# Performance work log

Measured on AMD Instinct MI355X. Metric: run time of the kernel, lower is better.

## Reference

```python
import jax, jax.numpy as jnp
import numpy as np

TEMPERATURE = 2.0
RAD2DEG = 180.0 / np.pi


def _safe_norm(diff, axis=-1):
    # L2 norm with zero (sub)gradient at 0, matching torch's convention and
    # avoiding NaNs on the (later-discarded) diagonal of pairwise distances.
    d2 = jnp.sum(diff * diff, axis=axis)
    pos = d2 > 0
    return jnp.where(pos, jnp.sqrt(jnp.where(pos, d2, 1.0)), 0.0)


def _rot6d_to_matrix(d6):
    # pytorch3d.transforms.rotation_6d_to_matrix: Gram-Schmidt on two 3-vectors.
    a1, a2 = d6[..., :3], d6[..., 3:6]
    b1 = a1 / jnp.linalg.norm(a1, axis=-1, keepdims=True)
    a2p = a2 - jnp.sum(b1 * a2, axis=-1, keepdims=True) * b1
    b2 = a2p / jnp.linalg.norm(a2p, axis=-1, keepdims=True)
    b3 = jnp.cross(b1, b2)
    return jnp.stack([b1, b2, b3], axis=-2)  # [n, 3, 3], rows b1,b2,b3


def _pose_error(pose):
    rot = _rot6d_to_matrix(pose[:, :6])                    # [n,3,3]
    div = jnp.power(jnp.linalg.det(rot), 1.0 / 3.0)[:, None, None]
    rot = rot / div
    t = pose[:, 6:]                                        # [n,3]
    # trace(rot_i @ rot_j^T) = sum_ab rot_i[a,b]*rot_j[a,b]
    r_trace = jnp.einsum('iab,jab->ij', rot, rot)          # [n,n]
    cos_theta = (r_trace - 1.0) / 2.0
    theta = jnp.arccos(jnp.clip(cos_theta, -1.0, 1.0)) * RAD2DEG
    shift = _safe_norm(t[:, None, :] - t[None, :, :]) * 100.0
    return theta, shift


def reference(features, labels):
    n = features.shape[0]
    theta_diffs, shift_diffs = _pose_error(labels)

    # FeatureSimilarity('l2'): -||f_i - f_j|| / t
    logits = -_safe_norm(features[:, None, :] - features[None, :, :]) / TEMPERATURE
    logits = logits - jax.lax.stop_gradient(jnp.max(logits, axis=1, keepdims=True))
    exp_logits = jnp.exp(logits)

    # Drop diagonal -> [n, n-1], preserving ascending column order (masked_select).
    cols = jnp.arange(n - 1)
    jidx = cols[None, :] + (cols[None, :] >= jnp.arange(n)[:, None]).astype(cols.dtype)
    take = lambda x: jnp.take_along_axis(x, jidx, axis=1)
    L = take(logits)          # [n, n-1]
    E = take(exp_logits)      # [n, n-1]
    TD = take(theta_diffs)    # [n, n-1]
    SD = take(shift_diffs)    # [n, n-1]

    # Vectorize the k-loop: M[i,k,j] = diffs[i,j] >= diffs[i,k]
    mt = TD[:, None, :] >= TD[:, :, None]                 # [n, n-1, n-1]
    ms = SD[:, None, :] >= SD[:, :, None]
    denom_t = jnp.sum(jnp.where(mt, E[:, None, :], 0.0), axis=-1)  # [n, n-1]
    denom_s = jnp.sum(jnp.where(ms, E[:, None, :], 0.0), axis=-1)

    pos_log_probs = (2.0 * L - jnp.log(denom_t) - jnp.log(denom_s)) / 2.0
    return -jnp.sum(pos_log_probs) / (n * (n - 1))


def setup_inputs() -> dict:
    key = jax.random.key(0)
    k1, k2 = jax.random.split(key)
    features = jax.random.normal(k1, (512, 256), dtype=jnp.float32)
    labels = jax.random.normal(k2, (512, 9), dtype=jnp.float32)
    return {"features": features, "labels": labels}
```

## Files before the change

### kernel.cpp

```cpp
#include <hip/hip_runtime.h>
#include <math.h>

#define N 512
#define D 256
#define ITILE 2
#define TPB 512

__constant__ float kRad2Deg = 57.29577951308232f;

__global__ void prep_kernel(const float* __restrict__ labels,
                            float* __restrict__ rot,
                            float* __restrict__ tvec) {
    int i = blockIdx.x * blockDim.x + threadIdx.x;
    if (i >= N) return;
    const float* p = labels + i * 9;
    float a1x = p[0], a1y = p[1], a1z = p[2];
    float a2x = p[3], a2y = p[4], a2z = p[5];
    float n1 = sqrtf(a1x * a1x + a1y * a1y + a1z * a1z);
    float b1x = a1x / n1, b1y = a1y / n1, b1z = a1z / n1;
    float dp = b1x * a2x + b1y * a2y + b1z * a2z;
    float cx = a2x - dp * b1x, cy = a2y - dp * b1y, cz = a2z - dp * b1z;
    float n2 = sqrtf(cx * cx + cy * cy + cz * cz);
    float b2x = cx / n2, b2y = cy / n2, b2z = cz / n2;
    float b3x = b1y * b2z - b1z * b2y;
    float b3y = b1z * b2x - b1x * b2z;
    float b3z = b1x * b2y - b1y * b2x;
    float det = b1x * (b2y * b3z - b2z * b3y)
              - b1y * (b2x * b3z - b2z * b3x)
              + b1z * (b2x * b3y - b2y * b3x);
    float inv = 1.0f / cbrtf(det);
    float* r = rot + i * 9;
    r[0] = b1x * inv; r[1] = b1y * inv; r[2] = b1z * inv;
    r[3] = b2x * inv; r[4] = b2y * inv; r[5] = b2z * inv;
    r[6] = b3x * inv; r[7] = b3y * inv; r[8] = b3z * inv;
    tvec[i * 3 + 0] = p[6];
    tvec[i * 3 + 1] = p[7];
    tvec[i * 3 + 2] = p[8];
}

__global__ __launch_bounds__(TPB) void fused_kernel(
        const float* __restrict__ f,
        const float* __restrict__ rot,
        const float* __restrict__ tvec,
        float* __restrict__ acc) {
    __shared__ __attribute__((aligned(16))) float lds_fi[ITILE * D];
    __shared__ __attribute__((aligned(16))) float E2[ITILE][N];
    __shared__ __attribute__((aligned(16))) float TD2[ITILE][N];
    __shared__ __attribute__((aligned(16))) float SD2[ITILE][N];
    __shared__ float red[TPB / 64];

    const int j  = threadIdx.x;
    const int i0 = blockIdx.x * ITILE;

    lds_fi[j] = f[i0 * D + j];
    __syncthreads();

    float d2[ITILE];
#pragma unroll
    for (int r = 0; r < ITILE; ++r) d2[r] = 0.0f;

    const float4* __restrict__ fj4 = (const float4*)(f + j * D);
#pragma unroll 8
    for (int kk = 0; kk < D / 4; ++kk) {
        float4 v = fj4[kk];
#pragma unroll
        for (int r = 0; r < ITILE; ++r) {
            const float4 fi = *(const float4*)&lds_fi[r * D + kk * 4];
            float dx = fi.x - v.x, dy = fi.y - v.y;
            float dz = fi.z - v.z, dw = fi.w - v.w;
            d2[r] += dx * dx + dy * dy + dz * dz + dw * dw;
        }
    }

    float rj[9];
#pragma unroll
    for (int c = 0; c < 9; ++c) rj[c] = rot[j * 9 + c];
    const float tjx = tvec[j * 3 + 0];
    const float tjy = tvec[j * 3 + 1];
    const float tjz = tvec[j * 3 + 2];

    float Lv[ITILE];
#pragma unroll
    for (int r = 0; r < ITILE; ++r) {
        const int i = i0 + r;
        float tr = 0.0f;
#pragma unroll
        for (int c = 0; c < 9; ++c) tr += rot[i * 9 + c] * rj[c];
        float ct = (tr - 1.0f) * 0.5f;
        ct = fminf(1.0f, fmaxf(-1.0f, ct));
        float theta = acosf(ct) * kRad2Deg;

        float dx = tvec[i * 3 + 0] - tjx;
        float dy = tvec[i * 3 + 1] - tjy;
        float dz = tvec[i * 3 + 2] - tjz;
        float sd2 = dx * dx + dy * dy + dz * dz;
        float shift = (sd2 > 0.0f ? sqrtf(sd2) : 0.0f) * 100.0f;

        float dist = (d2[r] > 0.0f ? sqrtf(d2[r]) : 0.0f);
        float L = -dist * 0.5f;
        float E = (j == i) ? 0.0f : expf(L);
        Lv[r] = L;
        E2[r][j]  = E;
        TD2[r][j] = theta;
        SD2[r][j] = shift;
    }
    __syncthreads();

    float vsum = 0.0f;
#pragma unroll
    for (int r = 0; r < ITILE; ++r) {
        const int i = i0 + r;
        if (j == i) continue;
        const float tdj = TD2[r][j];
        const float sdj = SD2[r][j];
        float dt = 0.0f, ds = 0.0f;
        for (int k = 0; k < N; k += 4) {
            float4 e4 = *(const float4*)&E2[r][k];
            float4 t4 = *(const float4*)&TD2[r][k];
            float4 s4 = *(const float4*)&SD2[r][k];
            dt += (t4.x >= tdj ? e4.x : 0.0f);
            dt += (t4.y >= tdj ? e4.y : 0.0f);
            dt += (t4.z >= tdj ? e4.z : 0.0f);
            dt += (t4.w >= tdj ? e4.w : 0.0f);
            ds += (s4.x >= sdj ? e4.x : 0.0f);
            ds += (s4.y >= sdj ? e4.y : 0.0f);
            ds += (s4.z >= sdj ? e4.z : 0.0f);
            ds += (s4.w >= sdj ? e4.w : 0.0f);
        }
        vsum += Lv[r] - 0.5f * (logf(dt) + logf(ds));
    }

#pragma unroll
    for (int off = 32; off > 0; off >>= 1) vsum += __shfl_down(vsum, off, 64);
    const int lane = j & 63, wid = j >> 6;
    if (lane == 0) red[wid] = vsum;
    __syncthreads();
    if (j == 0) {
        float s = 0.0f;
#pragma unroll
        for (int w = 0; w < TPB / 64; ++w) s += red[w];
        atomicAdd(acc, s);
    }
}

__global__ void finalize_kernel(const float* __restrict__ acc,
                                float* __restrict__ out) {
    out[0] = -acc[0] / (float)(N * (N - 1));
}

extern "C" void kernel_launch(void* const* d_in, const int* in_sizes, int n_in,
                              void* d_out, int out_size, void* d_ws, size_t ws_size,
                              hipStream_t stream) {
    const float* f      = (const float*)d_in[0];
    const float* labels = (const float*)d_in[1];
    float* out = (float*)d_out;
    float* ws  = (float*)d_ws;

    float* rot  = ws;
    float* tvec = ws + N * 9;
    float* acc  = ws + N * 12;

    hipMemsetAsync(acc, 0, sizeof(float), stream);
    prep_kernel<<<(N + 255) / 256, 256, 0, stream>>>(labels, rot, tvec);
    fused_kernel<<<N / ITILE, TPB, 0, stream>>>(f, rot, tvec, acc);
    finalize_kernel<<<1, 1, 0, stream>>>(acc, out);
}
```

Baseline: 56.01 us.

## Split fused kernel into row-data and denominator kernels via global scratch

The fused kernel is split in two. The first kernel writes the exp-logit, theta and shift matrices to global workspace and accumulates the logit sum. A second kernel with 1024 blocks of 256 threads computes the masked denominators per (i,j) from those matrices. The aim is more parallelism in the O(n^3) comparison phase than the 256 blocks of 512 threads allow. The cost is about 3 MB of extra global traffic, an extra launch, and reads from global/L2 instead of LDS in the inner loop.

```diff
diff --git a/kernel.cpp b/kernel.cpp
--- a/kernel.cpp
+++ b/kernel.cpp
@@ -5,6 +5,7 @@
 #define D 256
 #define ITILE 2
 #define TPB 512
+#define NPAIRS 261632.0f
 
 __constant__ float kRad2Deg = 57.29577951308232f;
 
@@ -38,15 +39,15 @@
     tvec[i * 3 + 2] = p[8];
 }
 
-__global__ __launch_bounds__(TPB) void fused_kernel(
+__global__ __launch_bounds__(TPB) void rowdata_kernel(
         const float* __restrict__ f,
         const float* __restrict__ rot,
         const float* __restrict__ tvec,
+        float* __restrict__ E,
+        float* __restrict__ TD,
+        float* __restrict__ SD,
         float* __restrict__ acc) {
     __shared__ __attribute__((aligned(16))) float lds_fi[ITILE * D];
-    __shared__ __attribute__((aligned(16))) float E2[ITILE][N];
-    __shared__ __attribute__((aligned(16))) float TD2[ITILE][N];
-    __shared__ __attribute__((aligned(16))) float SD2[ITILE][N];
     __shared__ float red[TPB / 64];
 
     const int j  = threadIdx.x;
@@ -79,7 +80,7 @@
     const float tjy = tvec[j * 3 + 1];
     const float tjz = tvec[j * 3 + 2];
 
-    float Lv[ITILE];
+    float lsum = 0.0f;
 #pragma unroll
     for (int r = 0; r < ITILE; ++r) {
         const int i = i0 + r;
@@ -98,42 +99,17 @@
 
         float dist = (d2[r] > 0.0f ? sqrtf(d2[r]) : 0.0f);
         float L = -dist * 0.5f;
-        float E = (j == i) ? 0.0f : expf(L);
-        Lv[r] = L;
-        E2[r][j]  = E;
-        TD2[r][j] = theta;
-        SD2[r][j] = shift;
-    }
-    __syncthreads();
-
-    float vsum = 0.0f;
-#pragma unroll
-    for (int r = 0; r < ITILE; ++r) {
-        const int i = i0 + r;
-        if (j == i) continue;
-        const float tdj = TD2[r][j];
-        const float sdj = SD2[r][j];
-        float dt = 0.0f, ds = 0.0f;
-        for (int k = 0; k < N; k += 4) {
-            float4 e4 = *(const float4*)&E2[r][k];
-            float4 t4 = *(const float4*)&TD2[r][k];
-            float4 s4 = *(const float4*)&SD2[r][k];
-            dt += (t4.x >= tdj ? e4.x : 0.0f);
-            dt += (t4.y >= tdj ? e4.y : 0.0f);
-            dt += (t4.z >= tdj ? e4.z : 0.0f);
-            dt += (t4.w >= tdj ? e4.w : 0.0f);
-            ds += (s4.x >= sdj ? e4.x : 0.0f);
-            ds += (s4.y >= sdj ? e4.y : 0.0f);
-            ds += (s4.z >= sdj ? e4.z : 0.0f);
-            ds += (s4.w >= sdj ? e4.w : 0.0f);
-        }
-        vsum += Lv[r] - 0.5f * (logf(dt) + logf(ds));
+        float Ev = (j == i) ? 0.0f : expf(L);
+        E[i * N + j]  = Ev;
+        TD[i * N + j] = theta;
+        SD[i * N + j] = shift;
+        lsum += L;
     }
 
 #pragma unroll
-    for (int off = 32; off > 0; off >>= 1) vsum += __shfl_down(vsum, off, 64);
+    for (int off = 32; off > 0; off >>= 1) lsum += __shfl_down(lsum, off, 64);
     const int lane = j & 63, wid = j >> 6;
-    if (lane == 0) red[wid] = vsum;
+    if (lane == 0) red[wid] = lsum;
     __syncthreads();
     if (j == 0) {
         float s = 0.0f;
@@ -143,9 +119,54 @@
     }
 }
 
+__global__ __launch_bounds__(256) void denom_kernel(
+        const float* __restrict__ E,
+        const float* __restrict__ TD,
+        const float* __restrict__ SD,
+        float* __restrict__ acc) {
+    __shared__ float red[4];
+    const int i = blockIdx.x >> 1;
+    const int j = ((blockIdx.x & 1) << 8) + threadIdx.x;
+
+    const float* __restrict__ er = E  + i * N;
+    const float* __restrict__ tr = TD + i * N;
+    const float* __restrict__ sr = SD + i * N;
+
+    const float tdj = tr[j];
+    const float sdj = sr[j];
+
+    float dt = 0.0f, ds = 0.0f;
+#pragma unroll 4
+    for (int k = 0; k < N; k += 4) {
+        const float4 e4 = *(const float4*)(er + k);
+        const float4 t4 = *(const float4*)(tr + k);
+        const float4 s4 = *(const float4*)(sr + k);
+        dt += (t4.x >= tdj) ? e4.x : 0.0f;
+        dt += (t4.y >= tdj) ? e4.y : 0.0f;
+        dt += (t4.z >= tdj) ? e4.z : 0.0f;
+        dt += (t4.w >= tdj) ? e4.w : 0.0f;
+        ds += (s4.x >= sdj) ? e4.x : 0.0f;
+        ds += (s4.y >= sdj) ? e4.y : 0.0f;
+        ds += (s4.z >= sdj) ? e4.z : 0.0f;
+        ds += (s4.w >= sdj) ? e4.w : 0.0f;
+    }
+
+    float v = (j == i) ? 0.0f : -0.5f * (logf(dt) + logf(ds));
+
+#pragma unroll
+    for (int off = 32; off > 0; off >>= 1) v += __shfl_down(v, off, 64);
+    const int lane = threadIdx.x & 63, wid = threadIdx.x >> 6;
+    if (lane == 0) red[wid] = v;
+    __syncthreads();
+    if (threadIdx.x == 0) {
+        float s = red[0] + red[1] + red[2] + red[3];
+        atomicAdd(acc, s);
+    }
+}
+
 __global__ void finalize_kernel(const float* __restrict__ acc,
                                 float* __restrict__ out) {
-    out[0] = -acc[0] / (float)(N * (N - 1));
+    out[0] = -acc[0] / NPAIRS;
 }
 
 extern "C" void kernel_launch(void* const* d_in, const int* in_sizes, int n_in,
@@ -157,11 +178,15 @@
     float* ws  = (float*)d_ws;
 
     float* rot  = ws;
-    float* tvec = ws + N * 9;
-    float* acc  = ws + N * 12;
+    float* tvec = rot + N * 9;
+    float* acc  = tvec + N * 3;
+    float* E    = acc + 4;
+    float* TD   = E + N * N;
+    float* SD   = TD + N * N;
 
     hipMemsetAsync(acc, 0, sizeof(float), stream);
     prep_kernel<<<(N + 255) / 256, 256, 0, stream>>>(labels, rot, tvec);
-    fused_kernel<<<N / ITILE, TPB, 0, stream>>>(f, rot, tvec, acc);
+    rowdata_kernel<<<N / ITILE, TPB, 0, stream>>>(f, rot, tvec, E, TD, SD, acc);
+    denom_kernel<<<N * 2, 256, 0, stream>>>(E, TD, SD, acc);
     finalize_kernel<<<1, 1, 0, stream>>>(acc, out);
 }
```

New measurement: 76.17 us. 1.36x slower.
